# Kernel tuning notes

Hardware: AMD Instinct MI355X
Metric: run time of the kernel (lower is better)

The kernel has to match this reference:

```python
import jax, jax.numpy as jnp
import numpy as np

SEM_DIM = 256
AC_DIM = 36
CODEBOOK_SIZE = 8192
FSQ_LEVELS = 21
COMMIT_COST = 0.25
HALF = (FSQ_LEVELS - 1) / 2.0  # 10.0
EPS = 0.001


def setup_inputs() -> dict:
    key = jax.random.key(0)
    k1, k2 = jax.random.split(key)
    z = jax.random.normal(k1, (8, SEM_DIM + AC_DIM, 4096), dtype=jnp.float32)
    lim = 1.0 / CODEBOOK_SIZE
    codebook = jax.random.uniform(k2, (CODEBOOK_SIZE, SEM_DIM), dtype=jnp.float32,
                                  minval=-lim, maxval=lim)
    return {"z": z, "codebook": codebook}


def _round_ste(x):
    return x + jax.lax.stop_gradient(jnp.round(x) - x)


def _vq(z_sem, codebook):
    # z_sem: (B, D, T), codebook: (K, D)
    B, D, T = z_sem.shape
    z_flat = jnp.transpose(z_sem, (0, 2, 1)).reshape(B * T, D)  # (N, D)
    # pairwise squared distances via matmul: ||z||^2 - 2 z.W^T + ||W||^2
    dists = (jnp.sum(z_flat * z_flat, axis=1, keepdims=True)
             - 2.0 * jnp.matmul(z_flat, codebook.T)
             + jnp.sum(codebook * codebook, axis=1)[None, :])  # (N, K)
    indices = jnp.argmin(dists, axis=1)  # (N,)
    z_q_flat = codebook[indices]  # (N, D) gather
    z_q = jnp.transpose(z_q_flat.reshape(B, T, D), (0, 2, 1))  # (B, D, T)
    codebook_loss = jnp.mean((z_q - jax.lax.stop_gradient(z_sem)) ** 2)
    commitment_loss = COMMIT_COST * jnp.mean((jax.lax.stop_gradient(z_q) - z_sem) ** 2)
    loss = codebook_loss + commitment_loss
    z_q_ste = z_sem + jax.lax.stop_gradient(z_q - z_sem)  # straight-through
    return z_q_ste, indices.reshape(B, T), loss


def _fsq(z_ac):
    z_b = jnp.tanh(z_ac) * (HALF + EPS)
    z_q = _round_ste(z_b)
    codes = jnp.clip((z_q + HALF).astype(jnp.int32), 0, FSQ_LEVELS - 1)
    return z_q, codes


def reference(z, codebook):
    z_sem = z[:, :SEM_DIM, :]
    z_ac = z[:, SEM_DIM:, :]
    z_sem_q, sem_indices, vq_loss = _vq(z_sem, codebook)
    z_ac_q, ac_codes = _fsq(z_ac)
    z_q = jnp.concatenate([z_sem_q, z_ac_q], axis=1)
    return (z_q, sem_indices, ac_codes, vq_loss, z_ac_q)
```

## Files before the change

kernel.cpp:

```cpp
#include <hip/hip_runtime.h>
#include <math.h>

#define BB 8
#define DSEM 256
#define DAC 36
#define DTOT 292
#define TT 4096
#define NCB 8192
#define NROWS (BB*TT)

static constexpr size_t O0 = 0;
static constexpr size_t O1 = 9568256;
static constexpr size_t O2 = 9601024;
static constexpr size_t O3 = 10780672;
static constexpr size_t O4 = 10780673;

static constexpr size_t WB_AH   = 0;
static constexpr size_t WB_BH   = 16777216;
static constexpr size_t WB_TMIN = 20971520;
static constexpr size_t WB_CBT  = 37748736;
static constexpr size_t WB_RN   = 46137344;
static constexpr size_t WB_CSQ  = 46268416;
static constexpr size_t WB_LOSS = 46301184;
static constexpr size_t WB_CNT  = 46301192;
static constexpr size_t WB_RN4  = 46301200;
static constexpr size_t WB_END  = 47349776;
static constexpr unsigned WL_CAP = 4194304;

typedef _Float16 f16x8 __attribute__((ext_vector_type(8)));
typedef __attribute__((ext_vector_type(4))) float f32x4;

__device__ __forceinline__ void gload_lds16(const void* g, void* lds) {
  __builtin_amdgcn_global_load_lds(
      (const __attribute__((address_space(1))) void*)g,
      (__attribute__((address_space(3))) void*)lds, 16, 0, 0);
}


__global__ __launch_bounds__(256) void k_fsq(const float* __restrict__ z,
                                             float* __restrict__ out) {
  int e = blockIdx.x * 256 + threadIdx.x;
  int b = e / (DAC * TT);
  int rem = e - b * (DAC * TT);
  int d = rem >> 12, t = rem & 4095;
  float zv = z[((size_t)(b * DTOT + DSEM + d) << 12) + t];
  float th = (float)tanh((double)zv);
  float zb = th * 10.001f;
  float zq = rintf(zb);
  int code = (int)(zq + 10.0f);
  code = code < 0 ? 0 : (code > 20 ? 20 : code);
  out[O0 + (((size_t)(b * DTOT + DSEM + d)) << 12) + t] = zq;
  out[O2 + e] = (float)code;
  out[O4 + e] = zq;
}


__global__ __launch_bounds__(256) void k_prepB2(const float* __restrict__ cb,
                                                _Float16* __restrict__ Bh,
                                                float* __restrict__ csq,
                                                float* __restrict__ cbT4,
                                                double* __restrict__ loss,
                                                unsigned* __restrict__ counters) {
  if (blockIdx.x == 0 && threadIdx.x == 0) {
    loss[0] = 0.0; counters[0] = 0u; counters[1] = 0u;
  }
  int e = blockIdx.x * 256 + threadIdx.x;
  float4 v = reinterpret_cast<const float4*>(cb)[e];
  union { _Float16 h[4]; short4 s4; } o;
  o.h[0] = (_Float16)(v.x * -32768.0f);
  o.h[1] = (_Float16)(v.y * -32768.0f);
  o.h[2] = (_Float16)(v.z * -32768.0f);
  o.h[3] = (_Float16)(v.w * -32768.0f);
  reinterpret_cast<short4*>(Bh)[e] = o.s4;
  float s = v.x * v.x + v.y * v.y + v.z * v.z + v.w * v.w;
  for (int off = 32; off; off >>= 1) s += __shfl_xor(s, off);
  if ((threadIdx.x & 63) == 0) csq[e >> 6] = s;
  int c = e & 31, r = e >> 5;
  int u = r >> 6, k4 = r & 63;
  int j = (u << 5) + c;
  float4 w = *reinterpret_cast<const float4*>(cb + (size_t)j * 256 + k4 * 4);
  reinterpret_cast<float4*>(cbT4)[e] = w;
}

__global__ __launch_bounds__(256) void k_prepA(const float* __restrict__ z,
                                               _Float16* __restrict__ Ah,
                                               float* __restrict__ outz,
                                               double* __restrict__ rn4) {
  __shared__ float tile[64][65];
  __shared__ double rpart[4][64];
  int bid = blockIdx.x;
  int tt = bid & 63, kt = (bid >> 6) & 3, b = bid >> 8;
  int k0 = kt * 64, t0 = tt * 64;
  int tid = threadIdx.x;
  #pragma unroll
  for (int i = 0; i < 16; ++i) {
    int flat = i * 256 + tid;
    int kk = flat >> 6, t2 = flat & 63;
    tile[kk][t2] = z[((size_t)(b * DTOT + k0 + kk) << 12) + t0 + t2];
  }
  __syncthreads();
  int q = tid >> 6, t2r = tid & 63;
  double acc = 0.0;
  #pragma unroll
  for (int r = 0; r < 16; ++r) {
    float v = tile[q * 16 + r][t2r];
    acc += (double)v * (double)v;
  }
  rpart[q][t2r] = acc;
  float* zTb = outz + (size_t)b * (DTOT * TT);
  #pragma unroll
  for (int i = 0; i < 16; ++i) {
    int flat = i * 256 + tid;
    int t2 = flat >> 6, kk = flat & 63;
    float v = tile[kk][t2];
    Ah[(size_t)(b * 4096 + t0 + t2) * 256 + k0 + kk] = (_Float16)v;
    zTb[(size_t)(t0 + t2) * 256 + k0 + kk] = v;
  }
  __syncthreads();
  if (tid < 64) {
    double s = ((rpart[0][tid] + rpart[1][tid]) + rpart[2][tid]) + rpart[3][tid];
    rn4[(size_t)kt * NROWS + (b << 12) + t0 + tid] = s;
  }
}

__global__ __launch_bounds__(256) void k_gemm(const _Float16* __restrict__ A,
                                              const _Float16* __restrict__ B,
                                              const float* __restrict__ csq,
                                              _Float16* __restrict__ tmin) {
  __shared__ char smraw[128 * 68 * 4];
  _Float16* As = (_Float16*)smraw;
  _Float16* Bs = (_Float16*)(smraw + 16384);
  float* red = (float*)smraw;
  const float SCALE = 6.103515625e-05f;

  int bid = blockIdx.x;
  int wg = (bid & 7) * 2048 + (bid >> 3);
  int mtile = wg >> 6, ntile = wg & 63;
  int rbase = mtile << 7, cbase = ntile << 7;
  int tid = threadIdx.x, lane = tid & 63, wid = tid >> 6;
  int wm = wid >> 1, wn = wid & 1;
  int l15 = lane & 15, l4 = lane >> 4;
  int sw = l15 & 7;

  f32x4 acc[4][4];
  #pragma unroll
  for (int mi = 0; mi < 4; ++mi)
    #pragma unroll
    for (int ni = 0; ni < 4; ++ni) acc[mi][ni] = (f32x4){0.f, 0.f, 0.f, 0.f};

  for (int kt = 0; kt < 4; ++kt) {
    int kb = kt << 6;
    __syncthreads();
    #pragma unroll
    for (int i = 0; i < 4; ++i) {
      int flat = (wid * 4 + i) * 64 + lane;
      int row = flat >> 3;
      int csrc = (flat & 7) ^ (row & 7);
      gload_lds16(A + (size_t)(rbase + row) * 256 + kb + (csrc << 3),
                  (char*)As + flat * 16);
      gload_lds16(B + (size_t)(cbase + row) * 256 + kb + (csrc << 3),
                  (char*)Bs + flat * 16);
    }
    __syncthreads();
    #pragma unroll
    for (int ks = 0; ks < 2; ++ks) {
      int off = ((((ks << 2) + l4) ^ sw) << 3);
      f16x8 af[4], bv[4];
      #pragma unroll
      for (int mi = 0; mi < 4; ++mi)
        af[mi] = *(const f16x8*)(As + ((wm * 64 + mi * 16 + l15) << 6) + off);
      #pragma unroll
      for (int ni = 0; ni < 4; ++ni)
        bv[ni] = *(const f16x8*)(Bs + ((wn * 64 + ni * 16 + l15) << 6) + off);
      #pragma unroll
      for (int mi = 0; mi < 4; ++mi)
        #pragma unroll
        for (int ni = 0; ni < 4; ++ni)
          acc[mi][ni] = __builtin_amdgcn_mfma_f32_16x16x32_f16(af[mi], bv[ni], acc[mi][ni], 0, 0, 0);
    }
  }

  float csv[4];
  #pragma unroll
  for (int ni = 0; ni < 4; ++ni) csv[ni] = csq[cbase + wn * 64 + ni * 16 + l15];

  __syncthreads();
  #pragma unroll
  for (int mi = 0; mi < 4; ++mi) {
    #pragma unroll
    for (int r = 0; r < 4; ++r) {
      int row = wm * 64 + mi * 16 + l4 * 4 + r;
      float v0 = fminf(fmaf(acc[mi][0][r], SCALE, csv[0]),
                       fmaf(acc[mi][1][r], SCALE, csv[1]));
      float v1 = fminf(fmaf(acc[mi][2][r], SCALE, csv[2]),
                       fmaf(acc[mi][3][r], SCALE, csv[3]));
      red[row * 68 + (wn * 2 + 0) * 16 + l15] = v0;
      red[row * 68 + (wn * 2 + 1) * 16 + l15] = v1;
    }
  }
  __syncthreads();
  if (tid < 128) {
    int row = tid;
    const float* rp = red + row * 68;
    union { _Float16 h[4]; short4 s; } uu;
    #pragma unroll
    for (int q = 0; q < 4; ++q) {
      float m = rp[q * 16];
      #pragma unroll
      for (int x = 1; x < 16; ++x) m = fminf(m, rp[q * 16 + x]);
      uu.h[q] = (_Float16)m;
    }
    *reinterpret_cast<short4*>(tmin + (size_t)(rbase + row) * 256 + ntile * 4) = uu.s;
  }
}

__global__ __launch_bounds__(256) void k_cand(const _Float16* __restrict__ tmin,
                                              const double* __restrict__ rn4,
                                              float* __restrict__ rn,
                                              unsigned* __restrict__ wl,
                                              unsigned* __restrict__ counter,
                                              unsigned long long* __restrict__ result) {
  __shared__ unsigned long long smask[16][4];
  __shared__ unsigned scnt[16];
  __shared__ unsigned soff[16];
  int tid = threadIdx.x;
  int wv = tid >> 6, lane = tid & 63;
  int row0 = blockIdx.x << 4;

  for (int rr = wv; rr < 16; rr += 4) {
    int row = row0 + rr;
    const _Float16* tp = tmin + (size_t)row * 256;
    float v[4];
    #pragma unroll
    for (int i = 0; i < 4; ++i) v[i] = (float)tp[i * 64 + lane];
    float g = fminf(fminf(v[0], v[1]), fminf(v[2], v[3]));
    #pragma unroll
    for (int off = 32; off; off >>= 1) g = fminf(g, __shfl_xor(g, off));
    float thr = g + 1.5e-4f;
    if (lane == 0) {
      result[row] = 0xFFFFFFFFFFFFFFFFULL;
      double s = ((rn4[row] + rn4[NROWS + row]) + rn4[2 * NROWS + row]) +
                 rn4[3 * NROWS + row];
      rn[row] = (float)s;
    }
    unsigned cnt = 0;
    #pragma unroll
    for (int i = 0; i < 4; ++i) {
      unsigned long long mask = __ballot(v[i] <= thr);
      if (lane == 0) smask[rr][i] = mask;
      cnt += (unsigned)__popcll(mask);
    }
    if (lane == 0) scnt[rr] = cnt;
  }
  __syncthreads();
  if (tid == 0) {
    unsigned tot = 0;
    #pragma unroll
    for (int r = 0; r < 16; ++r) { soff[r] = tot; tot += scnt[r]; }
    unsigned base = atomicAdd(counter, tot);
    #pragma unroll
    for (int r = 0; r < 16; ++r) soff[r] += base;
  }
  __syncthreads();
  for (int rr = wv; rr < 16; rr += 4) {
    int row = row0 + rr;
    unsigned off = soff[rr];
    unsigned acc = 0;
    #pragma unroll
    for (int i = 0; i < 4; ++i) {
      unsigned long long mask = smask[rr][i];
      bool c = (mask >> lane) & 1ULL;
      if (c) {
        unsigned rank = acc + (unsigned)__popcll(mask & ((1ULL << lane) - 1ULL));
        unsigned idx = off + rank;
        if (idx < WL_CAP) wl[idx] = ((unsigned)row << 8) | (unsigned)(i * 64 + lane);
      }
      acc += (unsigned)__popcll(mask);
    }
  }
}

__global__ __launch_bounds__(256) void k_scan(const float* __restrict__ zT,
                                              const float* __restrict__ cbT4,
                                              const float* __restrict__ csq,
                                              const float* __restrict__ rn,
                                              const unsigned* __restrict__ wl,
                                              const unsigned* __restrict__ counter,
                                              unsigned long long* __restrict__ result) {
  unsigned total = *counter;
  if (total > WL_CAP) total = WL_CAP;
  int tid = threadIdx.x;
  unsigned stride = gridDim.x * 8u;
  int gw = blockIdx.x * 4 + (tid >> 6);
  int half = (tid >> 5) & 1, l32 = tid & 31;
  for (unsigned it = (unsigned)(gw * 2 + half); it < total; it += stride) {
    unsigned e = wl[it];
    int row = (int)(e >> 8), u = (int)(e & 255u);
    int j = (u << 5) + l32;
    int b = row >> 12, t = row & 4095;
    const float4* zp = reinterpret_cast<const float4*>(
        zT + (size_t)b * (DTOT * TT) + (size_t)t * 256);
    const float4* cp = reinterpret_cast<const float4*>(cbT4) + ((u * 64) * 32 + l32);
    float an = rn[row], cq = csq[j];
    float m0 = 0.f, m1 = 0.f, m2 = 0.f, m3 = 0.f;
    #pragma unroll 8
    for (int k4 = 0; k4 < 64; ++k4) {
      float4 cv = cp[k4 * 32];
      float4 zv = zp[k4];
      m0 = fmaf(zv.x, cv.x, m0);
      m1 = fmaf(zv.y, cv.y, m1);
      m2 = fmaf(zv.z, cv.z, m2);
      m3 = fmaf(zv.w, cv.w, m3);
    }
    float m = (m0 + m1) + (m2 + m3);
    float d = (an - 2.f * m) + cq;
    unsigned long long pk =
        (((unsigned long long)__float_as_uint(d)) << 32) | (unsigned)j;
    #pragma unroll
    for (int off = 16; off; off >>= 1) {
      unsigned long long o = __shfl_xor(pk, off);
      if (o < pk) pk = o;
    }
    if (l32 == 0) atomicMin(result + row, pk);
  }
}

__global__ __launch_bounds__(256) void k_out(const float* __restrict__ z,
                                             const float* __restrict__ cb,
                                             const unsigned long long* __restrict__ result,
                                             float* __restrict__ out0,
                                             float* __restrict__ out1,
                                             double* __restrict__ loss,
                                             unsigned* __restrict__ done,
                                             float* __restrict__ out3) {
  __shared__ float zs[32][257];
  __shared__ float hsum[8];
  int bid = blockIdx.x;
  int tt = bid & 127, b = bid >> 7;
  int t0 = tt * 32;
  int tid = threadIdx.x;

  #pragma unroll
  for (int i = 0; i < 8; ++i) {
    int flat = i * 256 + tid;
    int d = flat >> 3, t4 = (flat & 7) * 4;
    float4 v = *reinterpret_cast<const float4*>(
        z + ((size_t)(b * DTOT + d) << 12) + t0 + t4);
    zs[t4 + 0][d] = v.x; zs[t4 + 1][d] = v.y;
    zs[t4 + 2][d] = v.z; zs[t4 + 3][d] = v.w;
  }
  __syncthreads();

  int hw = tid >> 5, l32 = tid & 31;
  float lsum = 0.f;
  #pragma unroll
  for (int p = 0; p < 4; ++p) {
    int t2 = p * 8 + hw;
    int row = (b << 12) + t0 + t2;
    unsigned j = (unsigned)(result[row] & 0xFFFFFFFFULL);
    if (l32 == 0) out1[row] = (float)j;
    const float4* cp = reinterpret_cast<const float4*>(cb + (size_t)j * 256);
    float4 c0 = cp[l32 * 2], c1 = cp[l32 * 2 + 1];
    int d0 = l32 * 8;
    float cs = 0.f, df;
    df = c0.x - zs[t2][d0 + 0]; cs = fmaf(df, df, cs); zs[t2][d0 + 0] = c0.x;
    df = c0.y - zs[t2][d0 + 1]; cs = fmaf(df, df, cs); zs[t2][d0 + 1] = c0.y;
    df = c0.z - zs[t2][d0 + 2]; cs = fmaf(df, df, cs); zs[t2][d0 + 2] = c0.z;
    df = c0.w - zs[t2][d0 + 3]; cs = fmaf(df, df, cs); zs[t2][d0 + 3] = c0.w;
    df = c1.x - zs[t2][d0 + 4]; cs = fmaf(df, df, cs); zs[t2][d0 + 4] = c1.x;
    df = c1.y - zs[t2][d0 + 5]; cs = fmaf(df, df, cs); zs[t2][d0 + 5] = c1.y;
    df = c1.z - zs[t2][d0 + 6]; cs = fmaf(df, df, cs); zs[t2][d0 + 6] = c1.z;
    df = c1.w - zs[t2][d0 + 7]; cs = fmaf(df, df, cs); zs[t2][d0 + 7] = c1.w;
    lsum += cs;
  }
  #pragma unroll
  for (int off = 16; off; off >>= 1) lsum += __shfl_xor(lsum, off);
  if (l32 == 0) hsum[hw] = lsum;
  __syncthreads();

  #pragma unroll
  for (int i = 0; i < 8; ++i) {
    int flat = i * 256 + tid;
    int d = flat >> 3, t4 = (flat & 7) * 4;
    float4 v;
    v.x = zs[t4 + 0][d]; v.y = zs[t4 + 1][d];
    v.z = zs[t4 + 2][d]; v.w = zs[t4 + 3][d];
    *reinterpret_cast<float4*>(
        out0 + ((size_t)(b * DTOT + d) << 12) + t0 + t4) = v;
  }

  if (tid == 0) {
    float tot = ((hsum[0] + hsum[1]) + (hsum[2] + hsum[3])) +
                ((hsum[4] + hsum[5]) + (hsum[6] + hsum[7]));
    atomicAdd(loss, (double)tot);
    __threadfence();
    unsigned old = atomicAdd(done, 1u);
    if (old == 1023u) {
      double total = atomicAdd(loss, 0.0);
      out3[0] = (float)(1.25 * total / 8388608.0);
    }
  }
}


__global__ __launch_bounds__(256) void k_csq(const float* __restrict__ cb,
                                             float* __restrict__ csq,
                                             double* __restrict__ loss,
                                             unsigned* __restrict__ counter) {
  if (blockIdx.x == 0 && threadIdx.x == 0) { loss[0] = 0.0; counter[0] = 0u; }
  int w = (blockIdx.x << 2) + (threadIdx.x >> 6);
  int lane = threadIdx.x & 63;
  float4 v = *reinterpret_cast<const float4*>(cb + (size_t)w * DSEM + lane * 4);
  float s = v.x * v.x + v.y * v.y + v.z * v.z + v.w * v.w;
  for (int off = 32; off; off >>= 1) s += __shfl_xor(s, off);
  if (lane == 0) csq[w] = s;
}

__global__ __launch_bounds__(256) void k_rn(const float* __restrict__ z,
                                            float* __restrict__ rn) {
  int r = blockIdx.x * 256 + threadIdx.x;
  int b = r >> 12, t = r & 4095;
  const float* p = z + ((size_t)(b * DTOT) << 12) + t;
  double acc = 0.0;
  #pragma unroll 8
  for (int d = 0; d < DSEM; ++d) {
    float v = p[(size_t)d << 12];
    acc += (double)v * (double)v;
  }
  rn[r] = (float)acc;
}

__global__ void k_fin(const double* __restrict__ loss, float* __restrict__ out3) {
  out3[0] = (float)(1.25 * loss[0] / 8388608.0);
}

__global__ __launch_bounds__(256) void k_vq(const float* __restrict__ z,
                                            const float* __restrict__ cb,
                                            const float* __restrict__ csq,
                                            const float* __restrict__ rn,
                                            float* __restrict__ pmin,
                                            int* __restrict__ pidx) {
  __shared__ float As[32][132];
  __shared__ float Bs[32][132];
  const int tid = threadIdx.x;
  const int tx = tid & 15, ty = tid >> 4;
  const int mb = blockIdx.x >> 2, s = blockIdx.x & 3;
  const int r0 = mb << 7;
  const int b = r0 >> 12, t0 = r0 & 4095;
  const int nbase = s * 2048;

  int mrow[8], jcol[8];
  #pragma unroll
  for (int i = 0; i < 4; ++i) {
    mrow[i] = ty * 4 + i;  mrow[i + 4] = 64 + ty * 4 + i;
    jcol[i] = tx * 4 + i;  jcol[i + 4] = 64 + tx * 4 + i;
  }
  float an[8];
  #pragma unroll
  for (int i = 0; i < 8; ++i) an[i] = rn[r0 + mrow[i]];

  float rmin[8]; int ridx[8];
  #pragma unroll
  for (int i = 0; i < 8; ++i) { rmin[i] = 3.402823466e38f; ridx[i] = 0; }

  for (int nc = 0; nc < 16; ++nc) {
    const int n0 = nbase + nc * 128;
    float acc[8][8];
    #pragma unroll
    for (int i = 0; i < 8; ++i)
      #pragma unroll
      for (int j = 0; j < 8; ++j) acc[i][j] = 0.f;

    for (int kc = 0; kc < 8; ++kc) {
      const int kb = kc << 5;
      __syncthreads();
      #pragma unroll
      for (int i = 0; i < 4; ++i) {
        int flat = i * 256 + tid;
        int k = flat >> 5, m4 = (flat & 31) << 2;
        float4 vv = *reinterpret_cast<const float4*>(
            z + ((size_t)(b * DTOT + kb + k) << 12) + t0 + m4);
        *reinterpret_cast<float4*>(&As[k][m4]) = vv;
      }
      #pragma unroll
      for (int i = 0; i < 4; ++i) {
        int flat = i * 256 + tid;
        int j = flat >> 3, k4 = (flat & 7) << 2;
        float4 vv = *reinterpret_cast<const float4*>(
            cb + ((size_t)(n0 + j) << 8) + kb + k4);
        Bs[k4 + 0][j] = vv.x; Bs[k4 + 1][j] = vv.y;
        Bs[k4 + 2][j] = vv.z; Bs[k4 + 3][j] = vv.w;
      }
      __syncthreads();
      #pragma unroll 8
      for (int k = 0; k < 32; ++k) {
        float a[8], bv[8];
        *reinterpret_cast<float4*>(&a[0]) = *reinterpret_cast<const float4*>(&As[k][ty * 4]);
        *reinterpret_cast<float4*>(&a[4]) = *reinterpret_cast<const float4*>(&As[k][64 + ty * 4]);
        *reinterpret_cast<float4*>(&bv[0]) = *reinterpret_cast<const float4*>(&Bs[k][tx * 4]);
        *reinterpret_cast<float4*>(&bv[4]) = *reinterpret_cast<const float4*>(&Bs[k][64 + tx * 4]);
        #pragma unroll
        for (int i = 0; i < 8; ++i)
          #pragma unroll
          for (int j = 0; j < 8; ++j) acc[i][j] = fmaf(a[i], bv[j], acc[i][j]);
      }
    }
    float cs[8];
    #pragma unroll
    for (int j = 0; j < 8; ++j) cs[j] = csq[n0 + jcol[j]];
    #pragma unroll
    for (int i = 0; i < 8; ++i) {
      #pragma unroll
      for (int j = 0; j < 8; ++j) {
        float d = (an[i] - 2.f * acc[i][j]) + cs[j];
        int jg = n0 + jcol[j];
        if (d < rmin[i] || (d == rmin[i] && jg < ridx[i])) { rmin[i] = d; ridx[i] = jg; }
      }
    }
  }
  __syncthreads();
  float* redf = &As[0][0];
  int* redi = reinterpret_cast<int*>(&Bs[0][0]);
  #pragma unroll
  for (int i = 0; i < 8; ++i) {
    redf[mrow[i] * 16 + tx] = rmin[i];
    redi[mrow[i] * 16 + tx] = ridx[i];
  }
  __syncthreads();
  if (tid < 128) {
    int row = tid;
    float bestv = redf[row * 16]; int bi = redi[row * 16];
    #pragma unroll
    for (int x = 1; x < 16; ++x) {
      float m = redf[row * 16 + x]; int ii = redi[row * 16 + x];
      if (m < bestv || (m == bestv && ii < bi)) { bestv = m; bi = ii; }
    }
    pmin[(size_t)(r0 + row) * 4 + s] = bestv;
    pidx[(size_t)(r0 + row) * 4 + s] = bi;
  }
}

__global__ __launch_bounds__(256) void k_comb(const float* __restrict__ pmin,
                                              const int* __restrict__ pidx,
                                              int* __restrict__ widx,
                                              float* __restrict__ out1) {
  int r = blockIdx.x * 256 + threadIdx.x;
  float best = pmin[r * 4]; int bi = pidx[r * 4];
  #pragma unroll
  for (int s2 = 1; s2 < 4; ++s2) {
    float m = pmin[r * 4 + s2]; int ii = pidx[r * 4 + s2];
    if (m < best || (m == best && ii < bi)) { best = m; bi = ii; }
  }
  widx[r] = bi;
  out1[r] = (float)bi;
}

__global__ __launch_bounds__(256) void k_loss_fb(const float* __restrict__ z,
                                                 const float* __restrict__ cb,
                                                 const int* __restrict__ idx,
                                                 float* __restrict__ out0,
                                                 double* __restrict__ loss) {
  float s = 0.f;
  for (int e = blockIdx.x * 256 + threadIdx.x; e < BB * DSEM * TT; e += 2048 * 256) {
    int b = e >> 20;
    int rem = e & 1048575;
    int d = rem >> 12, t = rem & 4095;
    int r = (b << 12) + t;
    int j = idx[r];
    float c = cb[(size_t)j * DSEM + d];
    size_t zi = ((size_t)(b * DTOT + d) << 12) + t;
    float zv = z[zi];
    out0[zi] = c;
    float df = c - zv;
    s += df * df;
  }
  for (int off = 32; off; off >>= 1) s += __shfl_xor(s, off);
  __shared__ float ws4[4];
  int lane = threadIdx.x & 63, w = threadIdx.x >> 6;
  if (lane == 0) ws4[w] = s;
  __syncthreads();
  if (threadIdx.x == 0) {
    float tot = ws4[0] + ws4[1] + ws4[2] + ws4[3];
    atomicAdd(loss, (double)tot);
  }
}


extern "C" void kernel_launch(void* const* d_in, const int* in_sizes, int n_in,
                              void* d_out, int out_size, void* d_ws, size_t ws_size,
                              hipStream_t stream) {
  const float* z  = (const float*)d_in[0];
  const float* cb = (const float*)d_in[1];
  float* out = (float*)d_out;

  if (ws_size >= WB_END) {
    char* wsb = (char*)d_ws;
    _Float16* Ah   = (_Float16*)(wsb + WB_AH);
    _Float16* Bh   = (_Float16*)(wsb + WB_BH);
    _Float16* tmin = (_Float16*)(wsb + WB_TMIN);
    float*    cbT4 = (float*)(wsb + WB_CBT);
    float*    rn   = (float*)(wsb + WB_RN);
    float*    csq  = (float*)(wsb + WB_CSQ);
    double*   loss = (double*)(wsb + WB_LOSS);
    unsigned* counters = (unsigned*)(wsb + WB_CNT);
    double*   rn4  = (double*)(wsb + WB_RN4);
    unsigned* wl = (unsigned*)(wsb + WB_AH);
    unsigned long long* result = (unsigned long long*)(wsb + WB_BH);
    float* zT = out + O0;

    k_prepB2<<<2048, 256, 0, stream>>>(cb, Bh, csq, cbT4, loss, counters);
    k_fsq<<<(BB * DAC * TT) / 256, 256, 0, stream>>>(z, out);
    k_prepA<<<2048, 256, 0, stream>>>(z, Ah, zT, rn4);
    k_gemm<<<16384, 256, 0, stream>>>(Ah, Bh, csq, tmin);
    k_cand<<<NROWS / 16, 256, 0, stream>>>(tmin, rn4, rn, wl, counters, result);
    k_scan<<<4096, 256, 0, stream>>>(zT, cbT4, csq, rn, wl, counters, result);
    k_out<<<1024, 256, 0, stream>>>(z, cb, result, out + O0, out + O1, loss,
                                    counters + 1, out + O3);
  } else {
    float* wsf = (float*)d_ws;
    float* csq  = wsf;
    float* rn   = wsf + 8192;
    float* pmin = wsf + 40960;
    int*   pidx = (int*)(wsf + 172032);
    int*   widx = (int*)(wsf + 303104);
    double* loss = (double*)(wsf + 335872);
    unsigned* counter = (unsigned*)(wsf + 335876);

    k_csq<<<NCB / 4, 256, 0, stream>>>(cb, csq, loss, counter);
    k_rn<<<NROWS / 256, 256, 0, stream>>>(z, rn);
    k_fsq<<<(BB * DAC * TT) / 256, 256, 0, stream>>>(z, out);
    k_vq<<<(NROWS / 128) * 4, 256, 0, stream>>>(z, cb, csq, rn, pmin, pidx);
    k_comb<<<NROWS / 256, 256, 0, stream>>>(pmin, pidx, widx, out + O1);
    k_loss_fb<<<2048, 256, 0, stream>>>(z, cb, widx, out + O0, loss);
    k_fin<<<1, 1, 0, stream>>>(loss, out + O3);
  }
}
```

Baseline: 366.5 us.

## Bucket-sort candidate worklist by codebook tile and vectorize prepA stores

k_cand now builds a histogram of candidate codebook tiles, and two new kernels (a prefix sum and an atomic scatter) reorder the worklist so entries sharing a codebook tile are adjacent. k_scan then processes contiguous chunks per block, so a block reuses the same codebook tile rows through cache. k_prepA is also restructured to load rows directly while accumulating norms, and it writes fp16 and fp32 transposed outputs as vector stores. In exchange, this adds two extra launches, global atomics in the scatter, and an extra pass over the worklist.

```diff
diff --git a/kernel.cpp b/kernel.cpp
--- a/kernel.cpp
+++ b/kernel.cpp
@@ -23,8 +23,10 @@
 static constexpr size_t WB_CSQ  = 46268416;
 static constexpr size_t WB_LOSS = 46301184;
 static constexpr size_t WB_CNT  = 46301192;
-static constexpr size_t WB_RN4  = 46301200;
-static constexpr size_t WB_END  = 47349776;
+static constexpr size_t WB_HIST = 46301200;
+static constexpr size_t WB_CUR  = 46302224;
+static constexpr size_t WB_RN4  = 46303248;
+static constexpr size_t WB_END  = 47351824;
 static constexpr unsigned WL_CAP = 4194304;
 
 typedef _Float16 f16x8 __attribute__((ext_vector_type(8)));
@@ -60,9 +62,11 @@
                                                 float* __restrict__ csq,
                                                 float* __restrict__ cbT4,
                                                 double* __restrict__ loss,
-                                                unsigned* __restrict__ counters) {
-  if (blockIdx.x == 0 && threadIdx.x == 0) {
-    loss[0] = 0.0; counters[0] = 0u; counters[1] = 0u;
+                                                unsigned* __restrict__ counters,
+                                                unsigned* __restrict__ ghist) {
+  if (blockIdx.x == 0) {
+    if (threadIdx.x == 0) { loss[0] = 0.0; counters[0] = 0u; counters[1] = 0u; }
+    ghist[threadIdx.x] = 0u;
   }
   int e = blockIdx.x * 256 + threadIdx.x;
   float4 v = reinterpret_cast<const float4*>(cb)[e];
@@ -92,31 +96,34 @@
   int tt = bid & 63, kt = (bid >> 6) & 3, b = bid >> 8;
   int k0 = kt * 64, t0 = tt * 64;
   int tid = threadIdx.x;
-  #pragma unroll
-  for (int i = 0; i < 16; ++i) {
-    int flat = i * 256 + tid;
-    int kk = flat >> 6, t2 = flat & 63;
-    tile[kk][t2] = z[((size_t)(b * DTOT + k0 + kk) << 12) + t0 + t2];
-  }
-  __syncthreads();
   int q = tid >> 6, t2r = tid & 63;
   double acc = 0.0;
   #pragma unroll
-  for (int r = 0; r < 16; ++r) {
-    float v = tile[q * 16 + r][t2r];
+  for (int i = 0; i < 16; ++i) {
+    int kk = i * 4 + q;
+    float v = z[((size_t)(b * DTOT + k0 + kk) << 12) + t0 + t2r];
+    tile[t2r][kk] = v;
     acc += (double)v * (double)v;
   }
   rpart[q][t2r] = acc;
+  __syncthreads();
   float* zTb = outz + (size_t)b * (DTOT * TT);
   #pragma unroll
-  for (int i = 0; i < 16; ++i) {
+  for (int i = 0; i < 4; ++i) {
     int flat = i * 256 + tid;
-    int t2 = flat >> 6, kk = flat & 63;
-    float v = tile[kk][t2];
-    Ah[(size_t)(b * 4096 + t0 + t2) * 256 + k0 + kk] = (_Float16)v;
-    zTb[(size_t)(t0 + t2) * 256 + k0 + kk] = v;
-  }
-  __syncthreads();
+    int t2 = flat >> 4, k4g = (flat & 15) << 2;
+    float f0 = tile[t2][k4g + 0], f1 = tile[t2][k4g + 1];
+    float f2 = tile[t2][k4g + 2], f3 = tile[t2][k4g + 3];
+    union { _Float16 h[4]; short4 s; } hh;
+    hh.h[0] = (_Float16)f0; hh.h[1] = (_Float16)f1;
+    hh.h[2] = (_Float16)f2; hh.h[3] = (_Float16)f3;
+    *reinterpret_cast<short4*>(
+        Ah + (size_t)(b * 4096 + t0 + t2) * 256 + k0 + k4g) = hh.s;
+    float4 ff;
+    ff.x = f0; ff.y = f1; ff.z = f2; ff.w = f3;
+    *reinterpret_cast<float4*>(
+        zTb + (size_t)(t0 + t2) * 256 + k0 + k4g) = ff;
+  }
   if (tid < 64) {
     double s = ((rpart[0][tid] + rpart[1][tid]) + rpart[2][tid]) + rpart[3][tid];
     rn4[(size_t)kt * NROWS + (b << 12) + t0 + tid] = s;
@@ -219,13 +226,16 @@
                                               float* __restrict__ rn,
                                               unsigned* __restrict__ wl,
                                               unsigned* __restrict__ counter,
+                                              unsigned* __restrict__ ghist,
                                               unsigned long long* __restrict__ result) {
   __shared__ unsigned long long smask[16][4];
   __shared__ unsigned scnt[16];
   __shared__ unsigned soff[16];
+  __shared__ unsigned lhist[256];
   int tid = threadIdx.x;
   int wv = tid >> 6, lane = tid & 63;
   int row0 = blockIdx.x << 4;
+  lhist[tid] = 0u;
 
   for (int rr = wv; rr < 16; rr += 4) {
     int row = row0 + rr;
@@ -273,10 +283,44 @@
       if (c) {
         unsigned rank = acc + (unsigned)__popcll(mask & ((1ULL << lane) - 1ULL));
         unsigned idx = off + rank;
-        if (idx < WL_CAP) wl[idx] = ((unsigned)row << 8) | (unsigned)(i * 64 + lane);
+        unsigned u = (unsigned)(i * 64 + lane);
+        if (idx < WL_CAP) wl[idx] = ((unsigned)row << 8) | u;
+        atomicAdd(&lhist[u], 1u);
       }
       acc += (unsigned)__popcll(mask);
     }
+  }
+  __syncthreads();
+  atomicAdd(&ghist[tid], lhist[tid]);
+}
+
+__global__ __launch_bounds__(256) void k_pref(const unsigned* __restrict__ ghist,
+                                              unsigned* __restrict__ gcur) {
+  __shared__ unsigned tmp[256];
+  int tid = threadIdx.x;
+  unsigned v = ghist[tid];
+  tmp[tid] = v;
+  __syncthreads();
+  for (int off = 1; off < 256; off <<= 1) {
+    unsigned add = (tid >= off) ? tmp[tid - off] : 0u;
+    __syncthreads();
+    tmp[tid] += add;
+    __syncthreads();
+  }
+  gcur[tid] = tmp[tid] - v;
+}
+
+__global__ __launch_bounds__(256) void k_scat(const unsigned* __restrict__ wl,
+                                              const unsigned* __restrict__ counter,
+                                              unsigned* __restrict__ gcur,
+                                              unsigned* __restrict__ swl) {
+  unsigned total = *counter;
+  if (total > WL_CAP) total = WL_CAP;
+  for (unsigned i = blockIdx.x * 256 + threadIdx.x; i < total;
+       i += gridDim.x * 256) {
+    unsigned e = wl[i];
+    unsigned pos = atomicAdd(&gcur[e & 255u], 1u);
+    if (pos < WL_CAP) swl[pos] = e;
   }
 }
 
@@ -284,17 +328,19 @@
                                               const float* __restrict__ cbT4,
                                               const float* __restrict__ csq,
                                               const float* __restrict__ rn,
-                                              const unsigned* __restrict__ wl,
+                                              const unsigned* __restrict__ swl,
                                               const unsigned* __restrict__ counter,
                                               unsigned long long* __restrict__ result) {
   unsigned total = *counter;
   if (total > WL_CAP) total = WL_CAP;
+  unsigned C = (total + gridDim.x - 1) / gridDim.x;
+  unsigned s0 = blockIdx.x * C;
+  unsigned s1 = s0 + C;
+  if (s1 > total) s1 = total;
   int tid = threadIdx.x;
-  unsigned stride = gridDim.x * 8u;
-  int gw = blockIdx.x * 4 + (tid >> 6);
-  int half = (tid >> 5) & 1, l32 = tid & 31;
-  for (unsigned it = (unsigned)(gw * 2 + half); it < total; it += stride) {
-    unsigned e = wl[it];
+  int sub = tid >> 5, l32 = tid & 31;
+  for (unsigned it = s0 + (unsigned)sub; it < s1; it += 8u) {
+    unsigned e = swl[it];
     int row = (int)(e >> 8), u = (int)(e & 255u);
     int j = (u << 5) + l32;
     int b = row >> 12, t = row & 4095;
@@ -603,17 +649,22 @@
     float*    csq  = (float*)(wsb + WB_CSQ);
     double*   loss = (double*)(wsb + WB_LOSS);
     unsigned* counters = (unsigned*)(wsb + WB_CNT);
+    unsigned* ghist = (unsigned*)(wsb + WB_HIST);
+    unsigned* gcur  = (unsigned*)(wsb + WB_CUR);
     double*   rn4  = (double*)(wsb + WB_RN4);
-    unsigned* wl = (unsigned*)(wsb + WB_AH);
+    unsigned* wl  = (unsigned*)(wsb + WB_AH);
+    unsigned* swl = (unsigned*)(wsb + WB_TMIN);
     unsigned long long* result = (unsigned long long*)(wsb + WB_BH);
     float* zT = out + O0;
 
-    k_prepB2<<<2048, 256, 0, stream>>>(cb, Bh, csq, cbT4, loss, counters);
+    k_prepB2<<<2048, 256, 0, stream>>>(cb, Bh, csq, cbT4, loss, counters, ghist);
     k_fsq<<<(BB * DAC * TT) / 256, 256, 0, stream>>>(z, out);
     k_prepA<<<2048, 256, 0, stream>>>(z, Ah, zT, rn4);
     k_gemm<<<16384, 256, 0, stream>>>(Ah, Bh, csq, tmin);
-    k_cand<<<NROWS / 16, 256, 0, stream>>>(tmin, rn4, rn, wl, counters, result);
-    k_scan<<<4096, 256, 0, stream>>>(zT, cbT4, csq, rn, wl, counters, result);
+    k_cand<<<NROWS / 16, 256, 0, stream>>>(tmin, rn4, rn, wl, counters, ghist, result);
+    k_pref<<<1, 256, 0, stream>>>(ghist, gcur);
+    k_scat<<<256, 256, 0, stream>>>(wl, counters, gcur, swl);
+    k_scan<<<2048, 256, 0, stream>>>(zT, cbT4, csq, rn, swl, counters, result);
     k_out<<<1024, 256, 0, stream>>>(z, cb, result, out + O0, out + O1, loss,
                                     counters + 1, out + O3);
   } else {
```

After: 415.8 us. 13.5% more time.
